# Performance work log

Hardware: AMD Instinct MI355X
Metric: run time of the kernel (lower is better)

Reference implementation:

```python
import jax, jax.numpy as jnp
import numpy as np

N_AB = 1024
N = 2049  # odd; alpha[N//2] == pi/2
H = 64


def setup_inputs() -> dict:
    key = jax.random.key(0)
    k0, k1, k2, k3, k4, k5 = jax.random.split(key, 6)
    alpha = jnp.linspace(0.0, jnp.pi, N).astype(jnp.float32)
    s = 0.3  # keep tanh in its active range
    w0 = jax.random.normal(k0, (N_AB, H, 1), jnp.float32) * s
    w1 = jax.random.normal(k1, (N_AB, H, H), jnp.float32) * s
    w2 = jax.random.normal(k2, (N_AB, 2, H), jnp.float32) * s
    b0 = jax.random.normal(k3, (N_AB, H), jnp.float32) * s
    b1 = jax.random.normal(k4, (N_AB, H), jnp.float32) * s
    # original init: last bias = sqrt(ab_initial) with ab_initial > 0
    b2 = jnp.sqrt(jax.random.uniform(k5, (N_AB, 2), jnp.float32, 0.5, 2.0))
    return dict(alpha=alpha, w0=w0, w1=w1, w2=w2, b0=b0, b1=b1, b2=b2)


def _mlp(x, w0, w1, w2, b0, b1, b2):
    # x: (N_ab, B, 1) -> (N_ab, B, 2); squared output as in the torch module
    h = jnp.tanh(jnp.einsum('Nij,NBj->NBi', w0, x) + b0[:, None, :])
    h = jnp.tanh(jnp.einsum('Nij,NBj->NBi', w1, h) + b1[:, None, :])
    out = jnp.einsum('Nij,NBj->NBi', w2, h) + b2[:, None, :]
    return out * out


def reference(alpha, w0, w1, w2, b0, b1, b2):
    n = alpha.shape[0]
    half = n // 2 + 1
    n_ab = w0.shape[0]
    ah = alpha[:half]                                   # (B,)
    x_in = jnp.broadcast_to(ah[None, :, None], (n_ab, half, 1))
    # torch's double-backward trick == forward-mode derivative wrt a uniform
    # scalar shift of the input, i.e. a single JVP with tangent ones.
    f = lambda x: _mlp(x, w0, w1, w2, b0, b1, b2)
    x, dab = jax.jvp(f, (x_in,), (jnp.ones_like(x_in),))
    a, b = x[..., 0], x[..., 1]
    da, db = dab[..., 0], dab[..., 1]
    ca = jnp.cos(ah)[None, :]
    sa = jnp.sin(ah)[None, :]
    xp = a * (ca - 1.0)
    yp = b * sa
    xpp = -a * sa + da * (ca - 1.0)
    ypp = b * ca + db * sa
    flip = lambda t: t[:, :-1][:, ::-1]                 # mirror without midpoint
    xp = jnp.concatenate([xp, 2.0 * xp[:, -1:] - flip(xp)], axis=1)
    yp = jnp.concatenate([yp, flip(yp)], axis=1)
    xpp = jnp.concatenate([xpp, flip(xpp)], axis=1)
    ypp = jnp.concatenate([ypp, -flip(ypp)], axis=1)
    return xp, yp, xpp, ypp
```

## Files before the change

kernel.cpp:

```cpp
#include <hip/hip_runtime.h>

#define N_AB  1024
#define NHALF 1025
#define NFULL 2049
#define HDIM  64
#define PLANE ((size_t)N_AB * NFULL)
#define C2L   2.8853900817779268f

typedef __bf16 bf16x8 __attribute__((ext_vector_type(8)));
typedef __bf16 bf16x4 __attribute__((ext_vector_type(4)));
typedef float  f32x4  __attribute__((ext_vector_type(4)));
typedef float  f32x2  __attribute__((ext_vector_type(2)));

#define MFMA16(A,B,C) __builtin_amdgcn_mfma_f32_16x16x32_bf16(A,B,C,0,0,0)

#define TBLIDX2(IX2,H2,OMH2) { \
    float _f0 = __builtin_amdgcn_fmed3f(IX2.x, 0.5f, 2047.0f); \
    float _f1 = __builtin_amdgcn_fmed3f(IX2.y, 0.5f, 2047.0f); \
    H2.x = s_tanh[(int)_f0]; \
    H2.y = s_tanh[(int)_f1]; \
    OMH2 = __builtin_elementwise_fma(-H2, H2, _k1); }

#define L1P(I0, WI2, BI2, WD2, BV, BT) { \
    f32x2 _ix = __builtin_elementwise_fma(WI2, x2, BI2); \
    f32x2 _h, _omh; TBLIDX2(_ix,_h,_omh) \
    f32x2 _bt = _omh * WD2; \
    BV[I0] = (__bf16)_h.x; BV[I0+1] = (__bf16)_h.y; \
    BT[I0] = (__bf16)_bt.x; BT[I0+1] = (__bf16)_bt.y; }

#define L2P(AVI2, AT2, W20_2, W21_2) { \
    f32x2 _h, _omh; TBLIDX2(AVI2,_h,_omh) \
    f32x2 _dh = _omh * (AT2); \
    pv0_2 = __builtin_elementwise_fma(W20_2, _h,  pv0_2); \
    pv1_2 = __builtin_elementwise_fma(W21_2, _h,  pv1_2); \
    pt0_2 = __builtin_elementwise_fma(W20_2, _dh, pt0_2); \
    pt1_2 = __builtin_elementwise_fma(W21_2, _dh, pt1_2); }

#define L2QUAD(AV,AT,WR0,WR1) \
    L2P(AV.xy, AT.xy, WR0.xy, WR1.xy) \
    L2P(AV.zw, AT.zw, WR0.zw, WR1.zw)

#define COMPUTE_TILE(P) \
    const f32x4 tg = s_trig[P]; \
    const float x = tg.x, sa = tg.y, cam1 = tg.z, ca = tg.w; \
    const f32x2 x2 = {x, x}; \
    bf16x8 bv0, bv1, bt0, bt1; \
    L1P(0, w0iA.xy, b0iA.xy, w0dA.xy, bv0, bt0) \
    L1P(2, w0iA.zw, b0iA.zw, w0dA.zw, bv0, bt0) \
    L1P(4, w0iB.xy, b0iB.xy, w0dB.xy, bv0, bt0) \
    L1P(6, w0iB.zw, b0iB.zw, w0dB.zw, bv0, bt0) \
    L1P(0, w0iC.xy, b0iC.xy, w0dC.xy, bv1, bt1) \
    L1P(2, w0iC.zw, b0iC.zw, w0dC.zw, bv1, bt1) \
    L1P(4, w0iD.xy, b0iD.xy, w0dD.xy, bv1, bt1) \
    L1P(6, w0iD.zw, b0iD.zw, w0dD.zw, bv1, bt1) \
    const f32x4 zz = {0.0f,0.0f,0.0f,0.0f}; \
    f32x4 av0 = MFMA16(A01,bv1,MFMA16(A00,bv0,b1i0)); \
    f32x4 av1 = MFMA16(A11,bv1,MFMA16(A10,bv0,b1i1)); \
    f32x4 av2 = MFMA16(A21,bv1,MFMA16(A20,bv0,b1i2)); \
    f32x4 av3 = MFMA16(A31,bv1,MFMA16(A30,bv0,b1i3)); \
    f32x4 at0 = MFMA16(A01,bt1,MFMA16(A00,bt0,zz)); \
    f32x4 at1 = MFMA16(A11,bt1,MFMA16(A10,bt0,zz)); \
    f32x4 at2 = MFMA16(A21,bt1,MFMA16(A20,bt0,zz)); \
    f32x4 at3 = MFMA16(A31,bt1,MFMA16(A30,bt0,zz)); \
    f32x2 pv0_2 = {0.0f,0.0f}, pv1_2 = {0.0f,0.0f}; \
    f32x2 pt0_2 = {0.0f,0.0f}, pt1_2 = {0.0f,0.0f}; \
    L2QUAD(av0,at0,w2a0,w2b0) \
    L2QUAD(av1,at1,w2a1,w2b1) \
    L2QUAD(av2,at2,w2a2,w2b2) \
    L2QUAD(av3,at3,w2a3,w2b3) \
    float pv0 = pv0_2.x + pv0_2.y, pv1 = pv1_2.x + pv1_2.y; \
    float pt0 = pt0_2.x + pt0_2.y, pt1 = pt1_2.x + pt1_2.y; \
    pv0 += __shfl_xor(pv0,16); pv0 += __shfl_xor(pv0,32); \
    pv1 += __shfl_xor(pv1,16); pv1 += __shfl_xor(pv1,32); \
    pt0 += __shfl_xor(pt0,16); pt0 += __shfl_xor(pt0,32); \
    pt1 += __shfl_xor(pt1,16); pt1 += __shfl_xor(pt1,32); \
    const float z0 = pv0 + b20, z1 = pv1 + b21; \
    const float aa = z0*z0, bb = z1*z1; \
    const float da = 2.0f*z0*pt0, db = 2.0f*z1*pt1; \
    const float xp = aa*cam1, yp = bb*sa; \
    const float xpp = fmaf(da,cam1,-(aa*sa)); \
    const float ypp = fmaf(bb,ca, db*sa);

__global__ void __launch_bounds__(256, 2) sofa_kernel(
    const float* __restrict__ alpha,
    const float* __restrict__ w0,
    const float* __restrict__ w1,
    const float* __restrict__ w2,
    const float* __restrict__ b0,
    const float* __restrict__ b1,
    const float* __restrict__ b2,
    float* __restrict__ out)
{
    __shared__ __align__(16) __bf16 w1s[HDIM * HDIM];
    __shared__ __align__(16) f32x4 s_trig[NHALF];
    __shared__ __align__(16) float s_tanh[2048];
    __shared__ float s_xplast;

    const int n    = blockIdx.x;
    const int tid  = threadIdx.x;
    const int lane = tid & 63;
    const int wid  = tid >> 6;
    const int col  = lane & 15;
    const int grp  = lane >> 4;

    const float* __restrict__ w0n = w0 + (size_t)n * HDIM;
    const float* __restrict__ b0n = b0 + (size_t)n * HDIM;
    const float* __restrict__ w1n = w1 + (size_t)n * HDIM * HDIM;
    const float* __restrict__ b1n = b1 + (size_t)n * HDIM;
    const float* __restrict__ w2n = w2 + (size_t)n * 2 * HDIM;
    const float* __restrict__ b2n = b2 + (size_t)n * 2;

    for (int e = tid; e < NHALF; e += 256) {
        const float xx = alpha[e];
        const float cc = __cosf(xx);
        f32x4 t; t.x = xx; t.y = __sinf(xx); t.z = cc - 1.0f; t.w = cc;
        s_trig[e] = t;
    }
    for (int e = tid; e < 2048; e += 256) {
        const float z = (float)(e - 1024) * 0.00390625f;
        const float ee = __builtin_amdgcn_exp2f(z * C2L);
        s_tanh[e] = fmaf(-2.0f, __builtin_amdgcn_rcpf(1.0f + ee), 1.0f);
    }
    for (int e4 = tid; e4 < (HDIM * HDIM) / 4; e4 += 256) {
        const int i = e4 >> 4, j4 = (e4 & 15) << 2;
        f32x4 v = ((const f32x4*)w1n)[e4];
        bf16x4 b;
        b[0] = (__bf16)(v.x * 256.0f); b[1] = (__bf16)(v.y * 256.0f);
        b[2] = (__bf16)(v.z * 256.0f); b[3] = (__bf16)(v.w * 256.0f);
        *(bf16x4*)&w1s[i * 64 + (((j4 >> 3) ^ (i & 7)) << 3) + (j4 & 7)] = b;
    }
    __syncthreads();

    const f32x2 _k1 = {1.0f, 1.0f};

    const int jb0 = grp * 8, jb1 = 32 + grp * 8;
    f32x4 w0iA = *(const f32x4*)(w0n + jb0);
    f32x4 w0iB = *(const f32x4*)(w0n + jb0 + 4);
    f32x4 w0iC = *(const f32x4*)(w0n + jb1);
    f32x4 w0iD = *(const f32x4*)(w0n + jb1 + 4);
    const f32x4 w0dA = w0iA * 0.00390625f;
    const f32x4 w0dB = w0iB * 0.00390625f;
    const f32x4 w0dC = w0iC * 0.00390625f;
    const f32x4 w0dD = w0iD * 0.00390625f;
    w0iA *= 256.0f; w0iB *= 256.0f; w0iC *= 256.0f; w0iD *= 256.0f;
    f32x4 b0iA = *(const f32x4*)(b0n + jb0);
    f32x4 b0iB = *(const f32x4*)(b0n + jb0 + 4);
    f32x4 b0iC = *(const f32x4*)(b0n + jb1);
    f32x4 b0iD = *(const f32x4*)(b0n + jb1 + 4);
    b0iA = b0iA * 256.0f + 1024.5f; b0iB = b0iB * 256.0f + 1024.5f;
    b0iC = b0iC * 256.0f + 1024.5f; b0iD = b0iD * 256.0f + 1024.5f;

    f32x4 b1i0 = *(const f32x4*)(b1n + 0  + grp * 4);
    f32x4 b1i1 = *(const f32x4*)(b1n + 16 + grp * 4);
    f32x4 b1i2 = *(const f32x4*)(b1n + 32 + grp * 4);
    f32x4 b1i3 = *(const f32x4*)(b1n + 48 + grp * 4);
    b1i0 = b1i0 * 256.0f + 1024.5f; b1i1 = b1i1 * 256.0f + 1024.5f;
    b1i2 = b1i2 * 256.0f + 1024.5f; b1i3 = b1i3 * 256.0f + 1024.5f;

    const f32x4 w2a0 = *(const f32x4*)(w2n + 0  + grp * 4);
    const f32x4 w2a1 = *(const f32x4*)(w2n + 16 + grp * 4);
    const f32x4 w2a2 = *(const f32x4*)(w2n + 32 + grp * 4);
    const f32x4 w2a3 = *(const f32x4*)(w2n + 48 + grp * 4);
    const f32x4 w2b0 = *(const f32x4*)(w2n + 64 + 0  + grp * 4);
    const f32x4 w2b1 = *(const f32x4*)(w2n + 64 + 16 + grp * 4);
    const f32x4 w2b2 = *(const f32x4*)(w2n + 64 + 32 + grp * 4);
    const f32x4 w2b3 = *(const f32x4*)(w2n + 64 + 48 + grp * 4);
    const float b20 = b2n[0], b21 = b2n[1];

    const bf16x8* w1v = (const bf16x8*)w1s;
    const int sw = col & 7;
#define AF(RT,KH) w1v[((RT)*16 + col)*8 + (((KH)*4 + grp) ^ sw)]
    const bf16x8 A00 = AF(0,0), A01 = AF(0,1), A10 = AF(1,0), A11 = AF(1,1);
    const bf16x8 A20 = AF(2,0), A21 = AF(2,1), A30 = AF(3,0), A31 = AF(3,1);

    const size_t obase = (size_t)grp * PLANE + (size_t)n * NFULL;

    if (wid == 0) {
        COMPUTE_TILE(1024)
        if (col == 0) {
            out[obase + 1024] = (grp == 0) ? xp : (grp == 1) ? yp : (grp == 2) ? xpp : ypp;
            if (grp == 0) s_xplast = xp;
        }
    }
    __syncthreads();
    const float xl2 = 2.0f * s_xplast;

    #pragma unroll 1
    for (int it = 0; it < 16; ++it) {
        const int p = ((it * 4 + wid) << 4) + col;
        COMPUTE_TILE(p)
        const float vdir = (grp == 0) ? xp : (grp == 1) ? yp : (grp == 2) ? xpp : ypp;
        const float vmir = (grp == 0) ? (xl2 - xp)
                         : (grp == 1) ? yp
                         : (grp == 2) ? xpp : -ypp;
        out[obase + p] = vdir;
        out[obase + (2048 - p)] = vmir;
    }
}

extern "C" void kernel_launch(void* const* d_in, const int* in_sizes, int n_in,
                              void* d_out, int out_size, void* d_ws, size_t ws_size,
                              hipStream_t stream) {
    const float* alpha = (const float*)d_in[0];
    const float* w0    = (const float*)d_in[1];
    const float* w1    = (const float*)d_in[2];
    const float* w2    = (const float*)d_in[3];
    const float* b0    = (const float*)d_in[4];
    const float* b1    = (const float*)d_in[5];
    const float* b2    = (const float*)d_in[6];
    float* out = (float*)d_out;
    sofa_kernel<<<dim3(N_AB), dim3(256), 0, stream>>>(alpha, w0, w1, w2, b0, b1, b2, out);
}
```

Measured before the change: 51.23 us.

## Compute output layer with MFMA and store tanh derivative in lookup table

Replaces the per-lane FMA accumulation and cross-lane shuffle reduction for the final 64->2 layer with two bf16 MFMAs per tile. The layer-2 activations are packed into bf16 fragments, and the w2 rows are zero-padded into an A-operand. The tanh table now also stores 1-h^2, so the FMA that computed it per element is gone. This trades VALU and shuffle work for extra MFMA issue and bf16 rounding of the last layer's inputs and weights.

```diff
diff --git a/kernel.cpp b/kernel.cpp
--- a/kernel.cpp
+++ b/kernel.cpp
@@ -14,36 +14,31 @@
 
 #define MFMA16(A,B,C) __builtin_amdgcn_mfma_f32_16x16x32_bf16(A,B,C,0,0,0)
 
-#define TBLIDX2(IX2,H2,OMH2) { \
+#define TBL2(IX2,H2,O2) { \
     float _f0 = __builtin_amdgcn_fmed3f(IX2.x, 0.5f, 2047.0f); \
     float _f1 = __builtin_amdgcn_fmed3f(IX2.y, 0.5f, 2047.0f); \
-    H2.x = s_tanh[(int)_f0]; \
-    H2.y = s_tanh[(int)_f1]; \
-    OMH2 = __builtin_elementwise_fma(-H2, H2, _k1); }
+    f32x2 _e0 = s_tanh2[(int)_f0]; \
+    f32x2 _e1 = s_tanh2[(int)_f1]; \
+    H2.x = _e0.x; H2.y = _e1.x; \
+    O2.x = _e0.y; O2.y = _e1.y; }
 
 #define L1P(I0, WI2, BI2, WD2, BV, BT) { \
     f32x2 _ix = __builtin_elementwise_fma(WI2, x2, BI2); \
-    f32x2 _h, _omh; TBLIDX2(_ix,_h,_omh) \
-    f32x2 _bt = _omh * WD2; \
+    f32x2 _h, _o; TBL2(_ix,_h,_o) \
+    f32x2 _bt = _o * WD2; \
     BV[I0] = (__bf16)_h.x; BV[I0+1] = (__bf16)_h.y; \
     BT[I0] = (__bf16)_bt.x; BT[I0+1] = (__bf16)_bt.y; }
 
-#define L2P(AVI2, AT2, W20_2, W21_2) { \
-    f32x2 _h, _omh; TBLIDX2(AVI2,_h,_omh) \
-    f32x2 _dh = _omh * (AT2); \
-    pv0_2 = __builtin_elementwise_fma(W20_2, _h,  pv0_2); \
-    pv1_2 = __builtin_elementwise_fma(W21_2, _h,  pv1_2); \
-    pt0_2 = __builtin_elementwise_fma(W20_2, _dh, pt0_2); \
-    pt1_2 = __builtin_elementwise_fma(W21_2, _dh, pt1_2); }
-
-#define L2QUAD(AV,AT,WR0,WR1) \
-    L2P(AV.xy, AT.xy, WR0.xy, WR1.xy) \
-    L2P(AV.zw, AT.zw, WR0.zw, WR1.zw)
+#define L2P(AVI2, AT2, FV, FT, I0) { \
+    f32x2 _h, _o; TBL2(AVI2,_h,_o) \
+    f32x2 _dh = _o * (AT2); \
+    FV[I0] = (__bf16)_h.x;  FV[I0+1] = (__bf16)_h.y; \
+    FT[I0] = (__bf16)_dh.x; FT[I0+1] = (__bf16)_dh.y; }
 
 #define COMPUTE_TILE(P) \
     const f32x4 tg = s_trig[P]; \
-    const float x = tg.x, sa = tg.y, cam1 = tg.z, ca = tg.w; \
-    const f32x2 x2 = {x, x}; \
+    const float sa = tg.y, cam1 = tg.z, ca = tg.w; \
+    const f32x2 x2 = {tg.x, tg.x}; \
     bf16x8 bv0, bv1, bt0, bt1; \
     L1P(0, w0iA.xy, b0iA.xy, w0dA.xy, bv0, bt0) \
     L1P(2, w0iA.zw, b0iA.zw, w0dA.zw, bv0, bt0) \
@@ -62,19 +57,21 @@
     f32x4 at1 = MFMA16(A11,bt1,MFMA16(A10,bt0,zz)); \
     f32x4 at2 = MFMA16(A21,bt1,MFMA16(A20,bt0,zz)); \
     f32x4 at3 = MFMA16(A31,bt1,MFMA16(A30,bt0,zz)); \
-    f32x2 pv0_2 = {0.0f,0.0f}, pv1_2 = {0.0f,0.0f}; \
-    f32x2 pt0_2 = {0.0f,0.0f}, pt1_2 = {0.0f,0.0f}; \
-    L2QUAD(av0,at0,w2a0,w2b0) \
-    L2QUAD(av1,at1,w2a1,w2b1) \
-    L2QUAD(av2,at2,w2a2,w2b2) \
-    L2QUAD(av3,at3,w2a3,w2b3) \
-    float pv0 = pv0_2.x + pv0_2.y, pv1 = pv1_2.x + pv1_2.y; \
-    float pt0 = pt0_2.x + pt0_2.y, pt1 = pt1_2.x + pt1_2.y; \
-    pv0 += __shfl_xor(pv0,16); pv0 += __shfl_xor(pv0,32); \
-    pv1 += __shfl_xor(pv1,16); pv1 += __shfl_xor(pv1,32); \
-    pt0 += __shfl_xor(pt0,16); pt0 += __shfl_xor(pt0,32); \
-    pt1 += __shfl_xor(pt1,16); pt1 += __shfl_xor(pt1,32); \
-    const float z0 = pv0 + b20, z1 = pv1 + b21; \
+    bf16x8 hv0, hv1, ht0, ht1; \
+    L2P(av0.xy, at0.xy, hv0, ht0, 0) \
+    L2P(av0.zw, at0.zw, hv0, ht0, 2) \
+    L2P(av1.xy, at1.xy, hv0, ht0, 4) \
+    L2P(av1.zw, at1.zw, hv0, ht0, 6) \
+    L2P(av2.xy, at2.xy, hv1, ht1, 0) \
+    L2P(av2.zw, at2.zw, hv1, ht1, 2) \
+    L2P(av3.xy, at3.xy, hv1, ht1, 4) \
+    L2P(av3.zw, at3.zw, hv1, ht1, 6) \
+    f32x4 pvq = MFMA16(W2F1, hv1, MFMA16(W2F0, hv0, c2f)); \
+    f32x4 ptq = MFMA16(W2F1, ht1, MFMA16(W2F0, ht0, zz)); \
+    const float z0  = __shfl(pvq[0], col); \
+    const float z1  = __shfl(pvq[1], col); \
+    const float pt0 = __shfl(ptq[0], col); \
+    const float pt1 = __shfl(ptq[1], col); \
     const float aa = z0*z0, bb = z1*z1; \
     const float da = 2.0f*z0*pt0, db = 2.0f*z1*pt1; \
     const float xp = aa*cam1, yp = bb*sa; \
@@ -93,7 +90,7 @@
 {
     __shared__ __align__(16) __bf16 w1s[HDIM * HDIM];
     __shared__ __align__(16) f32x4 s_trig[NHALF];
-    __shared__ __align__(16) float s_tanh[2048];
+    __shared__ __align__(16) f32x2 s_tanh2[2048];
     __shared__ float s_xplast;
 
     const int n    = blockIdx.x;
@@ -119,7 +116,9 @@
     for (int e = tid; e < 2048; e += 256) {
         const float z = (float)(e - 1024) * 0.00390625f;
         const float ee = __builtin_amdgcn_exp2f(z * C2L);
-        s_tanh[e] = fmaf(-2.0f, __builtin_amdgcn_rcpf(1.0f + ee), 1.0f);
+        const float th = fmaf(-2.0f, __builtin_amdgcn_rcpf(1.0f + ee), 1.0f);
+        f32x2 en; en.x = th; en.y = fmaf(-th, th, 1.0f);
+        s_tanh2[e] = en;
     }
     for (int e4 = tid; e4 < (HDIM * HDIM) / 4; e4 += 256) {
         const int i = e4 >> 4, j4 = (e4 & 15) << 2;
@@ -130,8 +129,6 @@
         *(bf16x4*)&w1s[i * 64 + (((j4 >> 3) ^ (i & 7)) << 3) + (j4 & 7)] = b;
     }
     __syncthreads();
-
-    const f32x2 _k1 = {1.0f, 1.0f};
 
     const int jb0 = grp * 8, jb1 = 32 + grp * 8;
     f32x4 w0iA = *(const f32x4*)(w0n + jb0);
@@ -157,15 +154,22 @@
     b1i0 = b1i0 * 256.0f + 1024.5f; b1i1 = b1i1 * 256.0f + 1024.5f;
     b1i2 = b1i2 * 256.0f + 1024.5f; b1i3 = b1i3 * 256.0f + 1024.5f;
 
-    const f32x4 w2a0 = *(const f32x4*)(w2n + 0  + grp * 4);
-    const f32x4 w2a1 = *(const f32x4*)(w2n + 16 + grp * 4);
-    const f32x4 w2a2 = *(const f32x4*)(w2n + 32 + grp * 4);
-    const f32x4 w2a3 = *(const f32x4*)(w2n + 48 + grp * 4);
-    const f32x4 w2b0 = *(const f32x4*)(w2n + 64 + 0  + grp * 4);
-    const f32x4 w2b1 = *(const f32x4*)(w2n + 64 + 16 + grp * 4);
-    const f32x4 w2b2 = *(const f32x4*)(w2n + 64 + 32 + grp * 4);
-    const f32x4 w2b3 = *(const f32x4*)(w2n + 64 + 48 + grp * 4);
-    const float b20 = b2n[0], b21 = b2n[1];
+    const float* __restrict__ w2row = w2n + (col < 2 ? col * HDIM : 0);
+    f32x4 qa = *(const f32x4*)(w2row + grp * 4);
+    f32x4 qb = *(const f32x4*)(w2row + 16 + grp * 4);
+    f32x4 qc = *(const f32x4*)(w2row + 32 + grp * 4);
+    f32x4 qd = *(const f32x4*)(w2row + 48 + grp * 4);
+    if (col >= 2) {
+        qa = (f32x4){0.0f,0.0f,0.0f,0.0f}; qb = qa; qc = qa; qd = qa;
+    }
+    bf16x8 W2F0, W2F1;
+    W2F0[0]=(__bf16)qa.x; W2F0[1]=(__bf16)qa.y; W2F0[2]=(__bf16)qa.z; W2F0[3]=(__bf16)qa.w;
+    W2F0[4]=(__bf16)qb.x; W2F0[5]=(__bf16)qb.y; W2F0[6]=(__bf16)qb.z; W2F0[7]=(__bf16)qb.w;
+    W2F1[0]=(__bf16)qc.x; W2F1[1]=(__bf16)qc.y; W2F1[2]=(__bf16)qc.z; W2F1[3]=(__bf16)qc.w;
+    W2F1[4]=(__bf16)qd.x; W2F1[5]=(__bf16)qd.y; W2F1[6]=(__bf16)qd.z; W2F1[7]=(__bf16)qd.w;
+
+    f32x4 c2f = {0.0f, 0.0f, 0.0f, 0.0f};
+    if (grp == 0) { c2f[0] = b2n[0]; c2f[1] = b2n[1]; }
 
     const bf16x8* w1v = (const bf16x8*)w1s;
     const int sw = col & 7;
```

New measurement: 48.42 us. 1.06x faster.
